# Kernel tuning notes

Measured on AMD Instinct MI355X. Metric: run time of the kernel, lower is better.

The kernel has to match this reference:

```python
import jax, jax.numpy as jnp
import numpy as np

B, P, ENC, DEC, ATT, EMB, V, MEM, TCAP = 64, 196, 2048, 512, 512, 512, 10000, 128, 22
T = TCAP - 1  # max decode length (caption_lengths - 1)


def setup_inputs() -> dict:
    key = jax.random.key(0)
    ks = iter(jax.random.split(key, 32))
    def w(shape, s=0.02):
        return (jax.random.normal(next(ks), shape, jnp.float32) * s)
    encoder_out = jax.random.normal(next(ks), (B, P, ENC), jnp.float32)
    encoded_captions = jax.random.randint(next(ks), (B, TCAP), 0, V)
    lens = np.sort(np.asarray(jax.random.randint(next(ks), (B,), 5, TCAP + 1)))[::-1].copy()
    lens[0] = TCAP  # ensure max(decode_lengths) == T
    caption_lengths = jnp.asarray(lens, jnp.int32)
    return {
        'encoder_out': encoder_out,
        'encoded_captions': encoded_captions,
        'caption_lengths': caption_lengths,
        'emb_table': w((V, EMB), 0.05),
        # Linear weights stored as [in, out] (torch W.T), so y = x @ W + b
        'W_enc': w((ENC, ATT)), 'b_enc': jnp.zeros((ATT,), jnp.float32),
        'W_dec': w((DEC, ATT)), 'b_dec': jnp.zeros((ATT,), jnp.float32),
        'W_full': w((ATT, 1)), 'b_full': jnp.zeros((1,), jnp.float32),
        'W_inith': w((ENC, DEC)), 'b_inith': jnp.zeros((DEC,), jnp.float32),
        'W_initc': w((ENC, DEC)), 'b_initc': jnp.zeros((DEC,), jnp.float32),
        'W_beta': w((DEC, ENC)), 'b_beta': jnp.zeros((ENC,), jnp.float32),
        # LSTMCell (torch gate order i, f, g, o), stored as [in, 4*dec]
        'W_ih': w((EMB + ENC, 4 * DEC)), 'b_ih': jnp.zeros((4 * DEC,), jnp.float32),
        'W_hh': w((DEC, 4 * DEC)), 'b_hh': jnp.zeros((4 * DEC,), jnp.float32),
        'memory_bank': jax.random.normal(next(ks), (MEM, DEC), jnp.float32),
        'W_fc': w((DEC, V)), 'b_fc': jnp.zeros((V,), jnp.float32),
    }


def _decode(encoder_out, encoded_captions, caption_lengths, emb_table,
            W_enc, b_enc, W_dec, b_dec, W_full, b_full,
            W_inith, b_inith, W_initc, b_initc, W_beta, b_beta,
            W_ih, b_ih, W_hh, b_hh, memory_bank, W_fc, b_fc):
    dec_len = caption_lengths - 1  # decode_lengths
    embs = emb_table[encoded_captions]                 # [B, TCAP, EMB]
    mean_enc = encoder_out.mean(axis=1)                # [B, ENC]
    h0 = mean_enc @ W_inith + b_inith
    c0 = mean_enc @ W_initc + b_initc
    att1 = encoder_out @ W_enc + b_enc                 # [B, P, ATT] precomputed

    x_seq = jnp.swapaxes(embs[:, :T, :], 0, 1)         # [T, B, EMB]
    mask_seq = jnp.arange(T)[:, None] < dec_len[None, :]  # [T, B]

    def step(carry, inp):
        h, c = carry
        x_t, m = inp                                   # [B,EMB], [B]
        # attention
        att2 = h @ W_dec + b_dec                       # [B, ATT]
        e = (jax.nn.relu(att1 + att2[:, None, :]) @ W_full)[..., 0] + b_full[0]  # [B, P]
        alpha = jax.nn.softmax(e, axis=1)
        awe = jnp.einsum('bpe,bp->be', encoder_out, alpha)  # [B, ENC]
        gate = jax.nn.sigmoid(h @ W_beta + b_beta)
        awe = gate * awe
        # LSTMCell
        xi = jnp.concatenate([x_t, awe], axis=1)
        gates = xi @ W_ih + b_ih + h @ W_hh + b_hh      # [B, 4*DEC]
        gi, gf, gg, go = jnp.split(gates, 4, axis=1)
        c_new = jax.nn.sigmoid(gf) * c + jax.nn.sigmoid(gi) * jnp.tanh(gg)
        h_new = jax.nn.sigmoid(go) * jnp.tanh(c_new)
        # hash memory
        sim = h_new @ memory_bank.T                    # [B, MEM]
        h_new = h_new + jax.nn.softmax(sim, axis=1) @ memory_bank
        # fc (dropout = identity in eval)
        preds = h_new @ W_fc + b_fc                    # [B, V]
        m2 = m[:, None]
        h = jnp.where(m2, h_new, h)
        c = jnp.where(m2, c_new, c)
        preds = jnp.where(m2, preds, 0.0)
        alpha = jnp.where(m2, alpha, 0.0)
        return (h, c), (preds, alpha)

    (_, _), (preds_seq, alpha_seq) = jax.lax.scan(step, (h0, c0), (x_seq, mask_seq))
    predictions = jnp.swapaxes(preds_seq, 0, 1)        # [B, T, V]
    alphas = jnp.swapaxes(alpha_seq, 0, 1)             # [B, T, P]
    return predictions, dec_len, alphas


def reference(encoder_out, encoded_captions, caption_lengths, emb_table,
              W_enc, b_enc, W_dec, b_dec, W_full, b_full,
              W_inith, b_inith, W_initc, b_initc, W_beta, b_beta,
              W_ih, b_ih, W_hh, b_hh, memory_bank, W_fc, b_fc):
    return _decode(encoder_out, encoded_captions, caption_lengths, emb_table,
                   W_enc, b_enc, W_dec, b_dec, W_full, b_full,
                   W_inith, b_inith, W_initc, b_initc, W_beta, b_beta,
                   W_ih, b_ih, W_hh, b_hh, memory_bank, W_fc, b_fc)
```

## Files before the change

kernel.cpp:

```cpp
#include <hip/hip_runtime.h>

#define BB   64
#define PP   196
#define ENCD 2048
#define DECD 512
#define VV   10000
#define TT   21
#define KIH  2560

typedef __attribute__((ext_vector_type(8))) short bf16x8;
typedef __attribute__((ext_vector_type(4))) float f32x4;

__device__ __forceinline__ float sigm(float x)   { return 1.f / (1.f + __expf(-x)); }
__device__ __forceinline__ float tanh_f(float x) { return 1.f - 2.f / (1.f + __expf(2.f * x)); }
__device__ __forceinline__ ushort f2bf(float x) {
    unsigned u = __float_as_uint(x);
    unsigned r = (u + 0x7FFFu + ((u >> 16) & 1u)) >> 16;
    return (ushort)r;
}
__device__ __forceinline__ float bf2f(short u) {
    return __uint_as_float(((unsigned)(ushort)u) << 16);
}
union U8 { float4 f4; ushort u[8]; };


__global__ void k_cvt(const float* __restrict__ in, ushort* __restrict__ out, int n4) {
    int i = blockIdx.x * 256 + threadIdx.x;
    if (i >= n4) return;
    float4 v = ((const float4*)in)[i];
    ushort4 o; o.x = f2bf(v.x); o.y = f2bf(v.y); o.z = f2bf(v.z); o.w = f2bf(v.w);
    ((ushort4*)out)[i] = o;
}

__global__ void k_mean16(const ushort* __restrict__ encB, float* __restrict__ mean) {
    int idx = blockIdx.x * 256 + threadIdx.x;
    int b = idx >> 10, e2 = idx & 1023;
    const uint* p = (const uint*)encB + (size_t)b * PP * 1024 + e2;
    float s0 = 0.f, s1 = 0.f;
    #pragma unroll 7
    for (int i = 0; i < PP; ++i) {
        uint v = p[(size_t)i * 1024];
        s0 += __uint_as_float(v << 16);
        s1 += __uint_as_float(v & 0xffff0000u);
    }
    mean[b * 2048 + e2 * 2]     = s0 * (1.f / 196.f);
    mean[b * 2048 + e2 * 2 + 1] = s1 * (1.f / 196.f);
}

__global__ __launch_bounds__(256) void k_ipart(const float* __restrict__ mean,
        const float* __restrict__ Wh, const float* __restrict__ Wc,
        float* __restrict__ ipart) {
    __shared__ alignas(16) float As[32][68];
    __shared__ alignas(16) float Bs[32][68];
    const int n0 = blockIdx.x * 64;
    const int kc = blockIdx.y;
    const int mat = blockIdx.z;
    const float* Bp = mat ? Wc : Wh;
    const int tid = threadIdx.x, tx = tid & 15, ty = tid >> 4;
    float acc[4][4] = {};
    for (int k0 = 0; k0 < 512; k0 += 32) {
        #pragma unroll
        for (int p = 0; p < 2; ++p) {
            int c = p * 256 + tid;
            int m = c >> 3, k4 = (c & 7) * 4;
            float4 v = *(const float4*)(mean + m * 2048 + kc * 512 + k0 + k4);
            As[k4 + 0][m] = v.x; As[k4 + 1][m] = v.y; As[k4 + 2][m] = v.z; As[k4 + 3][m] = v.w;
            int kb = c >> 4, n4 = (c & 15) * 4;
            float4 w = *(const float4*)(Bp + (size_t)(kc * 512 + k0 + kb) * 512 + n0 + n4);
            *(float4*)&Bs[kb][n4] = w;
        }
        __syncthreads();
        #pragma unroll 8
        for (int k = 0; k < 32; ++k) {
            float4 a = *(const float4*)&As[k][ty * 4];
            float4 b = *(const float4*)&Bs[k][tx * 4];
            float av[4] = {a.x, a.y, a.z, a.w}, bv[4] = {b.x, b.y, b.z, b.w};
            #pragma unroll
            for (int i = 0; i < 4; ++i)
                #pragma unroll
                for (int j = 0; j < 4; ++j) acc[i][j] += av[i] * bv[j];
        }
        __syncthreads();
    }
    #pragma unroll
    for (int i = 0; i < 4; ++i) {
        int m = ty * 4 + i;
        #pragma unroll
        for (int j = 0; j < 4; ++j) {
            int n = n0 + tx * 4 + j;
            ipart[((size_t)(mat * 4 + kc) * BB + m) * 512 + n] = acc[i][j];
        }
    }
}

__global__ void k_ifin(const float* __restrict__ ipart,
                       const float* __restrict__ bh, const float* __restrict__ bc,
                       float* __restrict__ h, float* __restrict__ c, ushort* __restrict__ hB) {
    int idx = blockIdx.x * 256 + threadIdx.x;
    int mat = idx >> 15, rem = idx & 32767;
    int b = rem >> 9, d = rem & 511;
    float s = 0.f;
    #pragma unroll
    for (int kc = 0; kc < 4; ++kc) s += ipart[((size_t)(mat * 4 + kc) * BB + b) * 512 + d];
    if (mat) c[rem] = s + bc[d];
    else { float v = s + bh[d]; h[rem] = v; hB[rem] = f2bf(v); }
}

__global__ __launch_bounds__(256) void k_tcvt_all(
        const float* __restrict__ Wenc, const float* __restrict__ Wdec,
        const float* __restrict__ Wbeta, const float* __restrict__ Whh,
        const float* __restrict__ Wih, const float* __restrict__ Wfc,
        ushort* __restrict__ WencT, ushort* __restrict__ WdecT,
        ushort* __restrict__ WbetaT, ushort* __restrict__ WhhT,
        ushort* __restrict__ WihT, ushort* __restrict__ WfcT) {
    __shared__ float lds[64 * 65];
    int l = blockIdx.x;
    const float* in; ushort* out; int K, N, KT;
    if (l < 256)       { in = Wenc;  out = WencT;  K = 2048; N = 512;   KT = 32; }
    else if (l < 320)  { l -= 256;  in = Wdec;  out = WdecT;  K = 512;  N = 512;   KT = 8; }
    else if (l < 576)  { l -= 320;  in = Wbeta; out = WbetaT; K = 512;  N = 2048;  KT = 8; }
    else if (l < 832)  { l -= 576;  in = Whh;   out = WhhT;   K = 512;  N = 2048;  KT = 8; }
    else if (l < 2112) { l -= 832;  in = Wih;   out = WihT;   K = KIH;  N = 2048;  KT = 40; }
    else               { l -= 2112; in = Wfc;   out = WfcT;   K = 512;  N = 10000; KT = 8; }
    const int k0 = (l % KT) * 64, n0 = (l / KT) * 64;
    const int tid = threadIdx.x;
    for (int i = tid; i < 4096; i += 256) {
        int kk = i >> 6, nn = i & 63;
        float v = 0.f;
        if (n0 + nn < N) v = in[(size_t)(k0 + kk) * N + n0 + nn];
        lds[nn * 65 + kk] = v;
    }
    __syncthreads();
    for (int i = tid; i < 4096; i += 256) {
        int nn = i >> 6, kk = i & 63;
        out[(size_t)(n0 + nn) * K + k0 + kk] = f2bf(lds[nn * 65 + kk]);
    }
}

__global__ __launch_bounds__(256) void k_att1_256(const ushort* __restrict__ A,
        const ushort* __restrict__ Bt, const float* __restrict__ bias,
        ushort* __restrict__ C) {
    __shared__ alignas(16) ushort As[64 * 64];
    __shared__ alignas(16) ushort Bs[256 * 64];
    const int n0 = blockIdx.x * 256;
    const int m0 = blockIdx.y * 64;
    const int tid = threadIdx.x, wid = tid >> 6, lane = tid & 63;
    f32x4 acc[4][4] = {};
    for (int k0 = 0; k0 < 2048; k0 += 64) {
        #pragma unroll
        for (int p = 0; p < 2; ++p) {
            int c = p * 256 + tid;
            int r = c >> 3, cc = c & 7;
            float4 v = *(const float4*)(A + (size_t)(m0 + r) * 2048 + k0 + cc * 8);
            *(float4*)(As + r * 64 + ((cc ^ (r & 7)) * 8)) = v;
        }
        #pragma unroll
        for (int p = 0; p < 8; ++p) {
            int c = p * 256 + tid;
            int r = c >> 3, cc = c & 7;
            float4 v = *(const float4*)(Bt + (size_t)(n0 + r) * 2048 + k0 + cc * 8);
            *(float4*)(Bs + r * 64 + ((cc ^ (r & 7)) * 8)) = v;
        }
        __syncthreads();
        #pragma unroll
        for (int kk = 0; kk < 2; ++kk) {
            int ci = kk * 4 + (lane >> 4);
            bf16x8 afrag[4], bfrag[4];
            #pragma unroll
            for (int m = 0; m < 4; ++m) {
                int row = m * 16 + (lane & 15);
                afrag[m] = *(const bf16x8*)(As + row * 64 + ((ci ^ (row & 7)) * 8));
            }
            #pragma unroll
            for (int n = 0; n < 4; ++n) {
                int col = wid * 64 + n * 16 + (lane & 15);
                bfrag[n] = *(const bf16x8*)(Bs + col * 64 + ((ci ^ (col & 7)) * 8));
            }
            #pragma unroll
            for (int m = 0; m < 4; ++m)
                #pragma unroll
                for (int n = 0; n < 4; ++n)
                    acc[m][n] = __builtin_amdgcn_mfma_f32_16x16x32_bf16(afrag[m], bfrag[n], acc[m][n], 0, 0, 0);
        }
        __syncthreads();
    }
    #pragma unroll
    for (int m = 0; m < 4; ++m) {
        int rb = m0 + m * 16 + (lane >> 4) * 4;
        #pragma unroll
        for (int n = 0; n < 4; ++n) {
            int col = n0 + wid * 64 + n * 16 + (lane & 15);
            float bv = bias[col];
            #pragma unroll
            for (int r = 0; r < 4; ++r)
                C[(size_t)(rb + r) * 512 + col] = f2bf(acc[m][n][r] + bv);
        }
    }
}

__global__ void k_declen(const int* __restrict__ lens, float* __restrict__ out) {
    int b = threadIdx.x;
    if (b < BB) out[b] = (float)(lens[b] - 1);
}


__global__ __launch_bounds__(256) void k_hgemm64(const ushort* __restrict__ hB,
        const float* __restrict__ emb, const int* __restrict__ caps, int t,
        const ushort* __restrict__ WdecT, const float* __restrict__ bd,
        const ushort* __restrict__ WbetaT, const float* __restrict__ bb,
        const ushort* __restrict__ WhhT, const ushort* __restrict__ WihT,
        float* __restrict__ att2, float* __restrict__ gate, float* __restrict__ hhp) {
    __shared__ alignas(16) ushort As[64 * 64];
    __shared__ alignas(16) ushort Bs[64 * 64];
    __shared__ int capsh[64];
    const int bx = blockIdx.x;
    int seg, n0;
    if (bx < 8)       { seg = 0; n0 = bx * 64; }
    else if (bx < 40) { seg = 1; n0 = (bx - 8) * 64; }
    else              { seg = 2; n0 = (bx - 40) * 64; }
    const int tid = threadIdx.x, wid = tid >> 6, lane = tid & 63;
    if (tid < 64) capsh[tid] = caps[tid * 22 + t];
    __syncthreads();
    const int KSEG = (seg == 2) ? 1024 : 512;
    f32x4 acc[4] = {};
    for (int k0 = 0; k0 < KSEG; k0 += 64) {
        const bool second = k0 >= 512;
        #pragma unroll
        for (int p = 0; p < 2; ++p) {
            int c = p * 256 + tid;
            int r = c >> 3, cc = c & 7;
            if (!second) {
                float4 v = *(const float4*)(hB + r * 512 + k0 + cc * 8);
                *(float4*)(As + r * 64 + ((cc ^ (r & 7)) * 8)) = v;
            } else {
                const float* er = emb + (size_t)capsh[r] * 512 + (k0 - 512) + cc * 8;
                float4 v0 = *(const float4*)er;
                float4 v1 = *(const float4*)(er + 4);
                U8 pk;
                pk.u[0] = f2bf(v0.x); pk.u[1] = f2bf(v0.y); pk.u[2] = f2bf(v0.z); pk.u[3] = f2bf(v0.w);
                pk.u[4] = f2bf(v1.x); pk.u[5] = f2bf(v1.y); pk.u[6] = f2bf(v1.z); pk.u[7] = f2bf(v1.w);
                *(float4*)(As + r * 64 + ((cc ^ (r & 7)) * 8)) = pk.f4;
            }
            const ushort* brow;
            if (seg == 0)      brow = WdecT + (size_t)(n0 + r) * 512 + k0 + cc * 8;
            else if (seg == 1) brow = WbetaT + (size_t)(n0 + r) * 512 + k0 + cc * 8;
            else brow = second ? (WihT + (size_t)(n0 + r) * KIH + (k0 - 512) + cc * 8)
                               : (WhhT + (size_t)(n0 + r) * 512 + k0 + cc * 8);
            float4 v = *(const float4*)brow;
            *(float4*)(Bs + r * 64 + ((cc ^ (r & 7)) * 8)) = v;
        }
        __syncthreads();
        #pragma unroll
        for (int kk = 0; kk < 2; ++kk) {
            int ci = kk * 4 + (lane >> 4);
            int colL = wid * 16 + (lane & 15);
            bf16x8 bfrag = *(const bf16x8*)(Bs + colL * 64 + ((ci ^ (colL & 7)) * 8));
            #pragma unroll
            for (int m = 0; m < 4; ++m) {
                int row = m * 16 + (lane & 15);
                bf16x8 afrag = *(const bf16x8*)(As + row * 64 + ((ci ^ (row & 7)) * 8));
                acc[m] = __builtin_amdgcn_mfma_f32_16x16x32_bf16(afrag, bfrag, acc[m], 0, 0, 0);
            }
        }
        __syncthreads();
    }
    int colL = wid * 16 + (lane & 15);
    int col = n0 + colL;
    #pragma unroll
    for (int m = 0; m < 4; ++m) {
        int rb = m * 16 + (lane >> 4) * 4;
        #pragma unroll
        for (int r = 0; r < 4; ++r) {
            int row = rb + r;
            float v = acc[m][r];
            if (seg == 0)      att2[row * 512 + col] = v + bd[col];
            else if (seg == 1) gate[row * 2048 + col] = sigm(v + bb[col]);
            else               hhp[(size_t)row * 2048 + col] = v;
        }
    }
}

__global__ __launch_bounds__(256) void k_escore_p(const ushort* __restrict__ att1B,
        const float* __restrict__ att2, const float* __restrict__ Wf,
        float* __restrict__ es) {
    __shared__ float a2[512], wf[512];
    int b = blockIdx.y, pc = blockIdx.x, tid = threadIdx.x;
    for (int i = tid; i < 512; i += 256) { a2[i] = att2[b * 512 + i]; wf[i] = Wf[i]; }
    __syncthreads();
    int lane = tid & 63, wid = tid >> 6;
    for (int i = wid; i < 49; i += 4) {
        int p = pc * 49 + i;
        bf16x8 rv = *(const bf16x8*)(att1B + ((size_t)(b * PP + p)) * 512 + lane * 8);
        float s = 0.f;
        #pragma unroll
        for (int j = 0; j < 8; ++j) {
            float v = bf2f(rv[j]) + a2[lane * 8 + j];
            s += (v > 0.f ? v : 0.f) * wf[lane * 8 + j];
        }
        #pragma unroll
        for (int off = 32; off; off >>= 1) s += __shfl_down(s, off);
        if (lane == 0) es[b * 256 + p] = s;
    }
}

__global__ __launch_bounds__(256) void k_awe16s(const ushort* __restrict__ encB,
        const float* __restrict__ es, const float* __restrict__ gate,
        const int* __restrict__ lens, int t,
        uint* __restrict__ aweB, float* __restrict__ out_alpha) {
    __shared__ float al[224], red[256];
    int b = blockIdx.y, pc = blockIdx.x, tid = threadIdx.x;
    float v = (tid < PP) ? es[b * 256 + tid] : -3.4e38f;
    red[tid] = v; __syncthreads();
    for (int s = 128; s; s >>= 1) { if (tid < s) red[tid] = fmaxf(red[tid], red[tid + s]); __syncthreads(); }
    float mx = red[0]; __syncthreads();
    float ev = (tid < PP) ? __expf(v - mx) : 0.f;
    red[tid] = ev; __syncthreads();
    for (int s = 128; s; s >>= 1) { if (tid < s) red[tid] += red[tid + s]; __syncthreads(); }
    float inv = 1.f / red[0];
    if (tid < PP) {
        float a = ev * inv;
        al[tid] = a;
        if (pc == 0) {
            bool m = t < (lens[b] - 1);
            out_alpha[((size_t)b * TT + t) * PP + tid] = m ? a : 0.f;
        }
    }
    __syncthreads();
    int pair = pc * 128 + (tid >> 1);
    int half = tid & 1;
    const uint* p = (const uint*)encB + (size_t)b * PP * 1024 + pair;
    float s0 = 0.f, s1 = 0.f;
    int i0 = half * 98;
    #pragma unroll 7
    for (int i = i0; i < i0 + 98; ++i) {
        uint vv = p[(size_t)i * 1024];
        float a = al[i];
        s0 += a * __uint_as_float(vv << 16);
        s1 += a * __uint_as_float(vv & 0xffff0000u);
    }
    s0 += __shfl_xor(s0, 1);
    s1 += __shfl_xor(s1, 1);
    if (half == 0) {
        int e = pair * 2;
        float g0 = s0 * gate[b * 2048 + e];
        float g1 = s1 * gate[b * 2048 + e + 1];
        aweB[b * 1024 + pair] = (uint)f2bf(g0) | ((uint)f2bf(g1) << 16);
    }
}

__global__ __launch_bounds__(256) void k_gawe64(const ushort* __restrict__ aweB,
        const ushort* __restrict__ WihT, float* __restrict__ pawe) {
    __shared__ alignas(16) ushort As[64 * 64];
    __shared__ alignas(16) ushort Bs[64 * 64];
    const int n0 = blockIdx.x * 64;
    const int kc = blockIdx.y;
    const int tid = threadIdx.x, wid = tid >> 6, lane = tid & 63;
    f32x4 acc[4] = {};
    for (int k0 = 0; k0 < 512; k0 += 64) {
        #pragma unroll
        for (int p = 0; p < 2; ++p) {
            int c = p * 256 + tid;
            int r = c >> 3, cc = c & 7;
            float4 v = *(const float4*)(aweB + r * 2048 + kc * 512 + k0 + cc * 8);
            *(float4*)(As + r * 64 + ((cc ^ (r & 7)) * 8)) = v;
            float4 w = *(const float4*)(WihT + (size_t)(n0 + r) * KIH + 512 + kc * 512 + k0 + cc * 8);
            *(float4*)(Bs + r * 64 + ((cc ^ (r & 7)) * 8)) = w;
        }
        __syncthreads();
        #pragma unroll
        for (int kk = 0; kk < 2; ++kk) {
            int ci = kk * 4 + (lane >> 4);
            int colL = wid * 16 + (lane & 15);
            bf16x8 bfrag = *(const bf16x8*)(Bs + colL * 64 + ((ci ^ (colL & 7)) * 8));
            #pragma unroll
            for (int m = 0; m < 4; ++m) {
                int row = m * 16 + (lane & 15);
                bf16x8 afrag = *(const bf16x8*)(As + row * 64 + ((ci ^ (row & 7)) * 8));
                acc[m] = __builtin_amdgcn_mfma_f32_16x16x32_bf16(afrag, bfrag, acc[m], 0, 0, 0);
            }
        }
        __syncthreads();
    }
    int col = n0 + wid * 16 + (lane & 15);
    #pragma unroll
    for (int m = 0; m < 4; ++m) {
        int rb = m * 16 + (lane >> 4) * 4;
        #pragma unroll
        for (int r = 0; r < 4; ++r)
            pawe[((size_t)kc * BB + rb + r) * 2048 + col] = acc[m][r];
    }
}

__global__ __launch_bounds__(256) void k_memattn(const float* __restrict__ hhp,
        const float* __restrict__ pawe,
        const float* __restrict__ bih, const float* __restrict__ bhh,
        const int* __restrict__ lens, int t, const float* __restrict__ memB,
        float* __restrict__ h, float* __restrict__ c,
        ushort* __restrict__ hB, ushort* __restrict__ histB) {
    __shared__ float hs[512], sims[128], red[256], ps[128];
    int b = blockIdx.x, tid = threadIdx.x;
    bool msk = t < (lens[b] - 1);
    for (int j = tid; j < 512; j += 256) {
        float g[4];
        #pragma unroll
        for (int q = 0; q < 4; ++q) {
            int col = q * 512 + j;
            float s = bih[col] + bhh[col] + hhp[(size_t)b * 2048 + col];
            #pragma unroll
            for (int kc = 0; kc < 4; ++kc) s += pawe[((size_t)kc * BB + b) * 2048 + col];
            g[q] = s;
        }
        float gi = sigm(g[0]), gf = sigm(g[1]), gg = tanh_f(g[2]), go = sigm(g[3]);
        float cold = c[b * 512 + j];
        float cn = gf * cold + gi * gg;
        c[b * 512 + j] = msk ? cn : cold;
        hs[j] = go * tanh_f(cn);
    }
    __syncthreads();
    int lane = tid & 63, wid = tid >> 6;
    for (int m = wid * 32; m < wid * 32 + 32; ++m) {
        const float* r = memB + (size_t)m * 512 + lane * 8;
        float4 r0 = *(const float4*)(r);
        float4 r1 = *(const float4*)(r + 4);
        float4 h0 = *(const float4*)(&hs[lane * 8]);
        float4 h1 = *(const float4*)(&hs[lane * 8 + 4]);
        float s = r0.x * h0.x + r0.y * h0.y + r0.z * h0.z + r0.w * h0.w
                + r1.x * h1.x + r1.y * h1.y + r1.z * h1.z + r1.w * h1.w;
        #pragma unroll
        for (int off = 32; off; off >>= 1) s += __shfl_down(s, off);
        if (lane == 0) sims[m] = s;
    }
    __syncthreads();
    float v = (tid < 128) ? sims[tid] : -3.4e38f;
    red[tid] = v; __syncthreads();
    for (int s = 128; s; s >>= 1) { if (tid < s) red[tid] = fmaxf(red[tid], red[tid + s]); __syncthreads(); }
    float mx = red[0]; __syncthreads();
    float ev = (tid < 128) ? __expf(v - mx) : 0.f;
    red[tid] = ev; __syncthreads();
    for (int s = 128; s; s >>= 1) { if (tid < s) red[tid] += red[tid + s]; __syncthreads(); }
    if (tid < 128) ps[tid] = ev / red[0];
    __syncthreads();
    for (int d = tid; d < 512; d += 256) {
        float s = 0.f;
        #pragma unroll 4
        for (int m = 0; m < 128; ++m) s += ps[m] * memB[(size_t)m * 512 + d];
        float hn = hs[d] + s;
        histB[((size_t)t * BB + b) * 512 + d] = f2bf(hn);
        float hold = h[b * 512 + d];
        float hv = msk ? hn : hold;
        h[b * 512 + d] = hv;
        hB[b * 512 + d] = f2bf(hv);
    }
}

__global__ __launch_bounds__(256) void k_preds_batch(const ushort* __restrict__ histB,
        const ushort* __restrict__ WfcT, const float* __restrict__ bfc,
        const int* __restrict__ lens, float* __restrict__ out) {
    __shared__ alignas(16) ushort As[64 * 64];
    __shared__ alignas(16) ushort Bs[256 * 64];
    const int n0 = blockIdx.x * 256;
    const int t = blockIdx.y;
    const ushort* A = histB + (size_t)t * BB * 512;
    const int tid = threadIdx.x, wid = tid >> 6, lane = tid & 63;
    f32x4 acc[4][4] = {};
    for (int k0 = 0; k0 < 512; k0 += 64) {
        #pragma unroll
        for (int p = 0; p < 2; ++p) {
            int c = p * 256 + tid;
            int r = c >> 3, cc = c & 7;
            float4 v = *(const float4*)(A + r * 512 + k0 + cc * 8);
            *(float4*)(As + r * 64 + ((cc ^ (r & 7)) * 8)) = v;
        }
        #pragma unroll
        for (int p = 0; p < 8; ++p) {
            int c = p * 256 + tid;
            int r = c >> 3, cc = c & 7;
            float4 v = *(const float4*)(WfcT + (size_t)(n0 + r) * 512 + k0 + cc * 8);
            *(float4*)(Bs + r * 64 + ((cc ^ (r & 7)) * 8)) = v;
        }
        __syncthreads();
        #pragma unroll
        for (int kk = 0; kk < 2; ++kk) {
            int ci = kk * 4 + (lane >> 4);
            bf16x8 afrag[4], bfrag[4];
            #pragma unroll
            for (int m = 0; m < 4; ++m) {
                int row = m * 16 + (lane & 15);
                afrag[m] = *(const bf16x8*)(As + row * 64 + ((ci ^ (row & 7)) * 8));
            }
            #pragma unroll
            for (int n = 0; n < 4; ++n) {
                int col = wid * 64 + n * 16 + (lane & 15);
                bfrag[n] = *(const bf16x8*)(Bs + col * 64 + ((ci ^ (col & 7)) * 8));
            }
            #pragma unroll
            for (int m = 0; m < 4; ++m)
                #pragma unroll
                for (int n = 0; n < 4; ++n)
                    acc[m][n] = __builtin_amdgcn_mfma_f32_16x16x32_bf16(afrag[m], bfrag[n], acc[m][n], 0, 0, 0);
        }
        __syncthreads();
    }
    #pragma unroll
    for (int m = 0; m < 4; ++m) {
        int rb = m * 16 + (lane >> 4) * 4;
        #pragma unroll
        for (int n = 0; n < 4; ++n) {
            int col = n0 + wid * 64 + n * 16 + (lane & 15);
            if (col < VV) {
                float bv = bfc[col];
                #pragma unroll
                for (int r = 0; r < 4; ++r) {
                    int b = rb + r;
                    bool msk = t < (lens[b] - 1);
                    out[((size_t)b * TT + t) * VV + col] = msk ? (acc[m][n][r] + bv) : 0.f;
                }
            }
        }
    }
}


extern "C" void kernel_launch(void* const* d_in, const int* in_sizes, int n_in,
                              void* d_out, int out_size, void* d_ws, size_t ws_size,
                              hipStream_t stream) {
    const float* enc     = (const float*)d_in[0];
    const int*   caps    = (const int*)d_in[1];
    const int*   lens    = (const int*)d_in[2];
    const float* emb     = (const float*)d_in[3];
    const float* W_enc   = (const float*)d_in[4];
    const float* b_enc   = (const float*)d_in[5];
    const float* W_dec   = (const float*)d_in[6];
    const float* b_dec   = (const float*)d_in[7];
    const float* W_full  = (const float*)d_in[8];
    const float* W_inith = (const float*)d_in[10];
    const float* b_inith = (const float*)d_in[11];
    const float* W_initc = (const float*)d_in[12];
    const float* b_initc = (const float*)d_in[13];
    const float* W_beta  = (const float*)d_in[14];
    const float* b_beta  = (const float*)d_in[15];
    const float* W_ih    = (const float*)d_in[16];
    const float* b_ih    = (const float*)d_in[17];
    const float* W_hh    = (const float*)d_in[18];
    const float* b_hh    = (const float*)d_in[19];
    const float* memB    = (const float*)d_in[20];
    const float* W_fc    = (const float*)d_in[21];
    const float* b_fc    = (const float*)d_in[22];

    float* out = (float*)d_out;
    float* preds_out  = out;
    float* declen_out = out + (size_t)BB * TT * VV;
    float* alpha_out  = declen_out + BB;

    float* ws    = (float*)d_ws;
    ushort* att1B = (ushort*)ws;        ws += (size_t)12544 * 512 / 2;
    float* h     = ws;  ws += BB * DECD;
    float* c     = ws;  ws += BB * DECD;
    float* att2  = ws;  ws += BB * 512;
    float* gate  = ws;  ws += BB * ENCD;
    float* es    = ws;  ws += BB * 256;
    float* hhp   = ws;  ws += BB * 2048;
    float* pawe  = ws;  ws += (size_t)4 * BB * 2048;
    ushort* hB   = (ushort*)ws;  ws += BB * DECD / 2;
    uint*  aweB  = (uint*)ws;    ws += BB * ENCD / 2;
    ushort* histB = (ushort*)ws; ws += (size_t)TT * BB * DECD / 2;
    ushort* encB  = (ushort*)ws; ws += (size_t)12544 * 2048 / 2;
    ushort* WencT = (ushort*)ws; ws += (size_t)512 * 2048 / 2;
    ushort* WfcT  = (ushort*)ws; ws += (size_t)10240 * 512 / 2;
    ushort* WdecT = (ushort*)ws; ws += (size_t)512 * 512 / 2;
    ushort* WbetaT= (ushort*)ws; ws += (size_t)2048 * 512 / 2;
    ushort* WhhT  = (ushort*)ws; ws += (size_t)2048 * 512 / 2;
    ushort* WihT  = (ushort*)ws; ws += (size_t)2048 * KIH / 2;
    float* ipart = hhp;
    float* mean  = (float*)att1B;

    k_cvt<<<(12544 * 2048 / 4 + 255) / 256, 256, 0, stream>>>(enc, encB, 12544 * 2048 / 4);
    k_mean16<<<256, 256, 0, stream>>>(encB, mean);
    k_ipart<<<dim3(8, 4, 2), 256, 0, stream>>>(mean, W_inith, W_initc, ipart);
    k_ifin<<<256, 256, 0, stream>>>(ipart, b_inith, b_initc, h, c, hB);
    k_declen<<<1, 64, 0, stream>>>(lens, declen_out);
    k_tcvt_all<<<3392, 256, 0, stream>>>(W_enc, W_dec, W_beta, W_hh, W_ih, W_fc,
                                         WencT, WdecT, WbetaT, WhhT, WihT, WfcT);
    k_att1_256<<<dim3(2, 196), 256, 0, stream>>>(encB, WencT, b_enc, att1B);

    for (int t = 0; t < TT; ++t) {
        k_hgemm64<<<72, 256, 0, stream>>>(hB, emb, caps, t, WdecT, b_dec, WbetaT, b_beta,
                                          WhhT, WihT, att2, gate, hhp);
        k_escore_p<<<dim3(4, 64), 256, 0, stream>>>(att1B, att2, W_full, es);
        k_awe16s<<<dim3(8, 64), 256, 0, stream>>>(encB, es, gate, lens, t, aweB, alpha_out);
        k_gawe64<<<dim3(32, 4), 256, 0, stream>>>((const ushort*)aweB, WihT, pawe);
        k_memattn<<<64, 256, 0, stream>>>(hhp, pawe, b_ih, b_hh, lens, t, memB, h, c, hB, histB);
    }
    k_preds_batch<<<dim3(40, TT), 256, 0, stream>>>(histB, WfcT, b_fc, lens, preds_out);
}
```

Before: 1.965 ms.

## Fuse per-step decode kernels into one cooperative persistent kernel with grid sync

Replaces the five per-timestep kernel launches with one cooperative persistent kernel that runs all 21 steps, separated by grid-wide syncs, and keeps a launch-per-phase fallback. The embedding part of the LSTM input projection is hoisted into a batched GEMM over all timesteps before the loop. The Wdec/Wbeta/Whh weights are concatenated into a single GEMM. att1 is stored transposed so the score and softmax/awe phases can be fused per batch row. The aim is to remove launch overhead and redundant per-step work. The cost is four grid barriers per step and a serial 512-length score loop per thread.

```diff
diff --git a/kernel.cpp b/kernel.cpp
--- a/kernel.cpp
+++ b/kernel.cpp
@@ -1,4 +1,7 @@
 #include <hip/hip_runtime.h>
+#include <hip/hip_cooperative_groups.h>
+
+namespace cg = cooperative_groups;
 
 #define BB   64
 #define PP   196
@@ -18,8 +21,8 @@
     unsigned r = (u + 0x7FFFu + ((u >> 16) & 1u)) >> 16;
     return (ushort)r;
 }
-__device__ __forceinline__ float bf2f(short u) {
-    return __uint_as_float(((unsigned)(ushort)u) << 16);
+__device__ __forceinline__ float bf2f(ushort u) {
+    return __uint_as_float(((unsigned)u) << 16);
 }
 union U8 { float4 f4; ushort u[8]; };
 
@@ -137,9 +140,9 @@
     }
 }
 
-__global__ __launch_bounds__(256) void k_att1_256(const ushort* __restrict__ A,
+__global__ __launch_bounds__(256) void k_att1T(const ushort* __restrict__ A,
         const ushort* __restrict__ Bt, const float* __restrict__ bias,
-        ushort* __restrict__ C) {
+        ushort* __restrict__ att1T) {
     __shared__ alignas(16) ushort As[64 * 64];
     __shared__ alignas(16) ushort Bs[256 * 64];
     const int n0 = blockIdx.x * 256;
@@ -187,13 +190,86 @@
     #pragma unroll
     for (int m = 0; m < 4; ++m) {
         int rb = m0 + m * 16 + (lane >> 4) * 4;
+        int b = rb / 196;
+        int p = rb - b * 196;
         #pragma unroll
         for (int n = 0; n < 4; ++n) {
             int col = n0 + wid * 64 + n * 16 + (lane & 15);
             float bv = bias[col];
+            ushort4 o;
+            o.x = f2bf(acc[m][n][0] + bv);
+            o.y = f2bf(acc[m][n][1] + bv);
+            o.z = f2bf(acc[m][n][2] + bv);
+            o.w = f2bf(acc[m][n][3] + bv);
+            *(ushort4*)(att1T + ((size_t)(b * 512 + col)) * 200 + p) = o;
+        }
+    }
+}
+
+__global__ __launch_bounds__(256) void k_xpre(const float* __restrict__ emb,
+        const int* __restrict__ caps, const ushort* __restrict__ WihT,
+        float* __restrict__ xpre) {
+    __shared__ alignas(16) ushort As[64 * 64];
+    __shared__ alignas(16) ushort Bs[256 * 64];
+    __shared__ int capsh[64];
+    const int n0 = blockIdx.x * 256;
+    const int t = blockIdx.y;
+    const int tid = threadIdx.x, wid = tid >> 6, lane = tid & 63;
+    if (tid < 64) capsh[tid] = caps[tid * 22 + t];
+    __syncthreads();
+    f32x4 acc[4][4] = {};
+    for (int k0 = 0; k0 < 512; k0 += 64) {
+        #pragma unroll
+        for (int p = 0; p < 2; ++p) {
+            int c = p * 256 + tid;
+            int r = c >> 3, cc = c & 7;
+            const float* er = emb + (size_t)capsh[r] * 512 + k0 + cc * 8;
+            float4 v0 = *(const float4*)er;
+            float4 v1 = *(const float4*)(er + 4);
+            U8 pk;
+            pk.u[0] = f2bf(v0.x); pk.u[1] = f2bf(v0.y); pk.u[2] = f2bf(v0.z); pk.u[3] = f2bf(v0.w);
+            pk.u[4] = f2bf(v1.x); pk.u[5] = f2bf(v1.y); pk.u[6] = f2bf(v1.z); pk.u[7] = f2bf(v1.w);
+            *(float4*)(As + r * 64 + ((cc ^ (r & 7)) * 8)) = pk.f4;
+        }
+        #pragma unroll
+        for (int p = 0; p < 8; ++p) {
+            int c = p * 256 + tid;
+            int r = c >> 3, cc = c & 7;
+            float4 v = *(const float4*)(WihT + (size_t)(n0 + r) * KIH + k0 + cc * 8);
+            *(float4*)(Bs + r * 64 + ((cc ^ (r & 7)) * 8)) = v;
+        }
+        __syncthreads();
+        #pragma unroll
+        for (int kk = 0; kk < 2; ++kk) {
+            int ci = kk * 4 + (lane >> 4);
+            bf16x8 afrag[4], bfrag[4];
+            #pragma unroll
+            for (int m = 0; m < 4; ++m) {
+                int row = m * 16 + (lane & 15);
+                afrag[m] = *(const bf16x8*)(As + row * 64 + ((ci ^ (row & 7)) * 8));
+            }
+            #pragma unroll
+            for (int n = 0; n < 4; ++n) {
+                int col = wid * 64 + n * 16 + (lane & 15);
+                bfrag[n] = *(const bf16x8*)(Bs + col * 64 + ((ci ^ (col & 7)) * 8));
+            }
+            #pragma unroll
+            for (int m = 0; m < 4; ++m)
+                #pragma unroll
+                for (int n = 0; n < 4; ++n)
+                    acc[m][n] = __builtin_amdgcn_mfma_f32_16x16x32_bf16(afrag[m], bfrag[n], acc[m][n], 0, 0, 0);
+        }
+        __syncthreads();
+    }
+    #pragma unroll
+    for (int m = 0; m < 4; ++m) {
+        int rb = m * 16 + (lane >> 4) * 4;
+        #pragma unroll
+        for (int n = 0; n < 4; ++n) {
+            int col = n0 + wid * 64 + n * 16 + (lane & 15);
             #pragma unroll
             for (int r = 0; r < 4; ++r)
-                C[(size_t)(rb + r) * 512 + col] = f2bf(acc[m][n][r] + bv);
+                xpre[((size_t)t * BB + rb + r) * 2048 + col] = acc[m][n][r];
         }
     }
 }
@@ -204,178 +280,49 @@
 }
 
 
-__global__ __launch_bounds__(256) void k_hgemm64(const ushort* __restrict__ hB,
-        const float* __restrict__ emb, const int* __restrict__ caps, int t,
-        const ushort* __restrict__ WdecT, const float* __restrict__ bd,
-        const ushort* __restrict__ WbetaT, const float* __restrict__ bb,
-        const ushort* __restrict__ WhhT, const ushort* __restrict__ WihT,
-        float* __restrict__ att2, float* __restrict__ gate, float* __restrict__ hhp) {
-    __shared__ alignas(16) ushort As[64 * 64];
-    __shared__ alignas(16) ushort Bs[64 * 64];
-    __shared__ int capsh[64];
-    const int bx = blockIdx.x;
-    int seg, n0;
-    if (bx < 8)       { seg = 0; n0 = bx * 64; }
-    else if (bx < 40) { seg = 1; n0 = (bx - 8) * 64; }
-    else              { seg = 2; n0 = (bx - 40) * 64; }
-    const int tid = threadIdx.x, wid = tid >> 6, lane = tid & 63;
-    if (tid < 64) capsh[tid] = caps[tid * 22 + t];
-    __syncthreads();
-    const int KSEG = (seg == 2) ? 1024 : 512;
+struct SArgs {
+    ushort* hB; float* h; float* c;
+    const ushort* WcatT; const float* bd; const float* bb;
+    const ushort* WihT; const float* xpre; const ushort* att1T;
+    const float* Wf; const ushort* encB;
+    const float* bih; const float* bhh;
+    const int* lens; const float* memB;
+    float* att2; float* gate; float* hhp;
+    uint* aweB; float* pawe;
+    ushort* histB; float* alpha_out;
+};
+
+struct SMem {
+    ushort As[64 * 64];
+    ushort Bs[64 * 64];
+    float a2s[512], wfs[512], reds[256], als[224];
+    float hss[512], simss[128], pss[128];
+};
+
+__device__ __forceinline__ void phase1(const SArgs& a, int bid, int tid, SMem& sm) {
+    const int lane = tid & 63, wid = tid >> 6;
+    const int n0 = bid * 64;
     f32x4 acc[4] = {};
-    for (int k0 = 0; k0 < KSEG; k0 += 64) {
-        const bool second = k0 >= 512;
+    for (int k0 = 0; k0 < 512; k0 += 64) {
         #pragma unroll
         for (int p = 0; p < 2; ++p) {
-            int c = p * 256 + tid;
-            int r = c >> 3, cc = c & 7;
-            if (!second) {
-                float4 v = *(const float4*)(hB + r * 512 + k0 + cc * 8);
-                *(float4*)(As + r * 64 + ((cc ^ (r & 7)) * 8)) = v;
-            } else {
-                const float* er = emb + (size_t)capsh[r] * 512 + (k0 - 512) + cc * 8;
-                float4 v0 = *(const float4*)er;
-                float4 v1 = *(const float4*)(er + 4);
-                U8 pk;
-                pk.u[0] = f2bf(v0.x); pk.u[1] = f2bf(v0.y); pk.u[2] = f2bf(v0.z); pk.u[3] = f2bf(v0.w);
-                pk.u[4] = f2bf(v1.x); pk.u[5] = f2bf(v1.y); pk.u[6] = f2bf(v1.z); pk.u[7] = f2bf(v1.w);
-                *(float4*)(As + r * 64 + ((cc ^ (r & 7)) * 8)) = pk.f4;
-            }
-            const ushort* brow;
-            if (seg == 0)      brow = WdecT + (size_t)(n0 + r) * 512 + k0 + cc * 8;
-            else if (seg == 1) brow = WbetaT + (size_t)(n0 + r) * 512 + k0 + cc * 8;
-            else brow = second ? (WihT + (size_t)(n0 + r) * KIH + (k0 - 512) + cc * 8)
-                               : (WhhT + (size_t)(n0 + r) * 512 + k0 + cc * 8);
-            float4 v = *(const float4*)brow;
-            *(float4*)(Bs + r * 64 + ((cc ^ (r & 7)) * 8)) = v;
+            int c8 = p * 256 + tid;
+            int r = c8 >> 3, cc = c8 & 7;
+            float4 v = *(const float4*)(a.hB + r * 512 + k0 + cc * 8);
+            *(float4*)(sm.As + r * 64 + ((cc ^ (r & 7)) * 8)) = v;
+            float4 w = *(const float4*)(a.WcatT + (size_t)(n0 + r) * 512 + k0 + cc * 8);
+            *(float4*)(sm.Bs + r * 64 + ((cc ^ (r & 7)) * 8)) = w;
         }
         __syncthreads();
         #pragma unroll
         for (int kk = 0; kk < 2; ++kk) {
             int ci = kk * 4 + (lane >> 4);
             int colL = wid * 16 + (lane & 15);
-            bf16x8 bfrag = *(const bf16x8*)(Bs + colL * 64 + ((ci ^ (colL & 7)) * 8));
+            bf16x8 bfrag = *(const bf16x8*)(sm.Bs + colL * 64 + ((ci ^ (colL & 7)) * 8));
             #pragma unroll
             for (int m = 0; m < 4; ++m) {
                 int row = m * 16 + (lane & 15);
-                bf16x8 afrag = *(const bf16x8*)(As + row * 64 + ((ci ^ (row & 7)) * 8));
-                acc[m] = __builtin_amdgcn_mfma_f32_16x16x32_bf16(afrag, bfrag, acc[m], 0, 0, 0);
-            }
-        }
-        __syncthreads();
-    }
-    int colL = wid * 16 + (lane & 15);
-    int col = n0 + colL;
-    #pragma unroll
-    for (int m = 0; m < 4; ++m) {
-        int rb = m * 16 + (lane >> 4) * 4;
-        #pragma unroll
-        for (int r = 0; r < 4; ++r) {
-            int row = rb + r;
-            float v = acc[m][r];
-            if (seg == 0)      att2[row * 512 + col] = v + bd[col];
-            else if (seg == 1) gate[row * 2048 + col] = sigm(v + bb[col]);
-            else               hhp[(size_t)row * 2048 + col] = v;
-        }
-    }
-}
-
-__global__ __launch_bounds__(256) void k_escore_p(const ushort* __restrict__ att1B,
-        const float* __restrict__ att2, const float* __restrict__ Wf,
-        float* __restrict__ es) {
-    __shared__ float a2[512], wf[512];
-    int b = blockIdx.y, pc = blockIdx.x, tid = threadIdx.x;
-    for (int i = tid; i < 512; i += 256) { a2[i] = att2[b * 512 + i]; wf[i] = Wf[i]; }
-    __syncthreads();
-    int lane = tid & 63, wid = tid >> 6;
-    for (int i = wid; i < 49; i += 4) {
-        int p = pc * 49 + i;
-        bf16x8 rv = *(const bf16x8*)(att1B + ((size_t)(b * PP + p)) * 512 + lane * 8);
-        float s = 0.f;
-        #pragma unroll
-        for (int j = 0; j < 8; ++j) {
-            float v = bf2f(rv[j]) + a2[lane * 8 + j];
-            s += (v > 0.f ? v : 0.f) * wf[lane * 8 + j];
-        }
-        #pragma unroll
-        for (int off = 32; off; off >>= 1) s += __shfl_down(s, off);
-        if (lane == 0) es[b * 256 + p] = s;
-    }
-}
-
-__global__ __launch_bounds__(256) void k_awe16s(const ushort* __restrict__ encB,
-        const float* __restrict__ es, const float* __restrict__ gate,
-        const int* __restrict__ lens, int t,
-        uint* __restrict__ aweB, float* __restrict__ out_alpha) {
-    __shared__ float al[224], red[256];
-    int b = blockIdx.y, pc = blockIdx.x, tid = threadIdx.x;
-    float v = (tid < PP) ? es[b * 256 + tid] : -3.4e38f;
-    red[tid] = v; __syncthreads();
-    for (int s = 128; s; s >>= 1) { if (tid < s) red[tid] = fmaxf(red[tid], red[tid + s]); __syncthreads(); }
-    float mx = red[0]; __syncthreads();
-    float ev = (tid < PP) ? __expf(v - mx) : 0.f;
-    red[tid] = ev; __syncthreads();
-    for (int s = 128; s; s >>= 1) { if (tid < s) red[tid] += red[tid + s]; __syncthreads(); }
-    float inv = 1.f / red[0];
-    if (tid < PP) {
-        float a = ev * inv;
-        al[tid] = a;
-        if (pc == 0) {
-            bool m = t < (lens[b] - 1);
-            out_alpha[((size_t)b * TT + t) * PP + tid] = m ? a : 0.f;
-        }
-    }
-    __syncthreads();
-    int pair = pc * 128 + (tid >> 1);
-    int half = tid & 1;
-    const uint* p = (const uint*)encB + (size_t)b * PP * 1024 + pair;
-    float s0 = 0.f, s1 = 0.f;
-    int i0 = half * 98;
-    #pragma unroll 7
-    for (int i = i0; i < i0 + 98; ++i) {
-        uint vv = p[(size_t)i * 1024];
-        float a = al[i];
-        s0 += a * __uint_as_float(vv << 16);
-        s1 += a * __uint_as_float(vv & 0xffff0000u);
-    }
-    s0 += __shfl_xor(s0, 1);
-    s1 += __shfl_xor(s1, 1);
-    if (half == 0) {
-        int e = pair * 2;
-        float g0 = s0 * gate[b * 2048 + e];
-        float g1 = s1 * gate[b * 2048 + e + 1];
-        aweB[b * 1024 + pair] = (uint)f2bf(g0) | ((uint)f2bf(g1) << 16);
-    }
-}
-
-__global__ __launch_bounds__(256) void k_gawe64(const ushort* __restrict__ aweB,
-        const ushort* __restrict__ WihT, float* __restrict__ pawe) {
-    __shared__ alignas(16) ushort As[64 * 64];
-    __shared__ alignas(16) ushort Bs[64 * 64];
-    const int n0 = blockIdx.x * 64;
-    const int kc = blockIdx.y;
-    const int tid = threadIdx.x, wid = tid >> 6, lane = tid & 63;
-    f32x4 acc[4] = {};
-    for (int k0 = 0; k0 < 512; k0 += 64) {
-        #pragma unroll
-        for (int p = 0; p < 2; ++p) {
-            int c = p * 256 + tid;
-            int r = c >> 3, cc = c & 7;
-            float4 v = *(const float4*)(aweB + r * 2048 + kc * 512 + k0 + cc * 8);
-            *(float4*)(As + r * 64 + ((cc ^ (r & 7)) * 8)) = v;
-            float4 w = *(const float4*)(WihT + (size_t)(n0 + r) * KIH + 512 + kc * 512 + k0 + cc * 8);
-            *(float4*)(Bs + r * 64 + ((cc ^ (r & 7)) * 8)) = w;
-        }
-        __syncthreads();
-        #pragma unroll
-        for (int kk = 0; kk < 2; ++kk) {
-            int ci = kk * 4 + (lane >> 4);
-            int colL = wid * 16 + (lane & 15);
-            bf16x8 bfrag = *(const bf16x8*)(Bs + colL * 64 + ((ci ^ (colL & 7)) * 8));
-            #pragma unroll
-            for (int m = 0; m < 4; ++m) {
-                int row = m * 16 + (lane & 15);
-                bf16x8 afrag = *(const bf16x8*)(As + row * 64 + ((ci ^ (row & 7)) * 8));
+                bf16x8 afrag = *(const bf16x8*)(sm.As + row * 64 + ((ci ^ (row & 7)) * 8));
                 acc[m] = __builtin_amdgcn_mfma_f32_16x16x32_bf16(afrag, bfrag, acc[m], 0, 0, 0);
             }
         }
@@ -386,71 +333,188 @@
     for (int m = 0; m < 4; ++m) {
         int rb = m * 16 + (lane >> 4) * 4;
         #pragma unroll
+        for (int r = 0; r < 4; ++r) {
+            int row = rb + r;
+            float v = acc[m][r];
+            if (col < 512)       a.att2[row * 512 + col] = v + a.bd[col];
+            else if (col < 2560) a.gate[row * 2048 + (col - 512)] = sigm(v + a.bb[col - 512]);
+            else                 a.hhp[(size_t)row * 2048 + (col - 2560)] = v;
+        }
+    }
+}
+
+__device__ __forceinline__ void phase2(const SArgs& a, int t, int bid, int tid, SMem& sm) {
+    const int b = bid >> 2, pc = bid & 3;
+    for (int i = tid; i < 512; i += 256) { sm.a2s[i] = a.att2[b * 512 + i]; sm.wfs[i] = a.Wf[i]; }
+    __syncthreads();
+    float es = -3.4e38f;
+    if (tid < PP) {
+        const ushort* rp = a.att1T + (size_t)b * 512 * 200 + tid;
+        float s = 0.f;
+        #pragma unroll 4
+        for (int k = 0; k < 512; ++k) {
+            float v = bf2f(rp[(size_t)k * 200]) + sm.a2s[k];
+            s += (v > 0.f ? v : 0.f) * sm.wfs[k];
+        }
+        es = s;
+    }
+    sm.reds[tid] = es; __syncthreads();
+    for (int s = 128; s; s >>= 1) { if (tid < s) sm.reds[tid] = fmaxf(sm.reds[tid], sm.reds[tid + s]); __syncthreads(); }
+    float mx = sm.reds[0]; __syncthreads();
+    float ev = (tid < PP) ? __expf(es - mx) : 0.f;
+    sm.reds[tid] = ev; __syncthreads();
+    for (int s = 128; s; s >>= 1) { if (tid < s) sm.reds[tid] += sm.reds[tid + s]; __syncthreads(); }
+    float inv = 1.f / sm.reds[0];
+    if (tid < PP) {
+        float al = ev * inv;
+        sm.als[tid] = al;
+        if (pc == 0) {
+            bool m = t < (a.lens[b] - 1);
+            a.alpha_out[((size_t)b * TT + t) * PP + tid] = m ? al : 0.f;
+        }
+    }
+    __syncthreads();
+    int pair = pc * 256 + tid;
+    const uint* pp = (const uint*)a.encB + (size_t)b * PP * 1024 + pair;
+    float s0 = 0.f, s1 = 0.f;
+    #pragma unroll 4
+    for (int i = 0; i < PP; ++i) {
+        uint vv = pp[(size_t)i * 1024];
+        float al = sm.als[i];
+        s0 += al * __uint_as_float(vv << 16);
+        s1 += al * __uint_as_float(vv & 0xffff0000u);
+    }
+    int e = pair * 2;
+    float g0 = s0 * a.gate[b * 2048 + e];
+    float g1 = s1 * a.gate[b * 2048 + e + 1];
+    a.aweB[b * 1024 + pair] = (uint)f2bf(g0) | ((uint)f2bf(g1) << 16);
+}
+
+__device__ __forceinline__ void phase3(const SArgs& a, int bid, int tid, SMem& sm) {
+    const int lane = tid & 63, wid = tid >> 6;
+    const int n0 = (bid & 31) * 64, kc = bid >> 5;
+    const ushort* aweU = (const ushort*)a.aweB;
+    f32x4 acc[4] = {};
+    for (int k0 = 0; k0 < 512; k0 += 64) {
+        #pragma unroll
+        for (int p = 0; p < 2; ++p) {
+            int c8 = p * 256 + tid;
+            int r = c8 >> 3, cc = c8 & 7;
+            float4 v = *(const float4*)(aweU + r * 2048 + kc * 512 + k0 + cc * 8);
+            *(float4*)(sm.As + r * 64 + ((cc ^ (r & 7)) * 8)) = v;
+            float4 w = *(const float4*)(a.WihT + (size_t)(n0 + r) * KIH + 512 + kc * 512 + k0 + cc * 8);
+            *(float4*)(sm.Bs + r * 64 + ((cc ^ (r & 7)) * 8)) = w;
+        }
+        __syncthreads();
+        #pragma unroll
+        for (int kk = 0; kk < 2; ++kk) {
+            int ci = kk * 4 + (lane >> 4);
+            int colL = wid * 16 + (lane & 15);
+            bf16x8 bfrag = *(const bf16x8*)(sm.Bs + colL * 64 + ((ci ^ (colL & 7)) * 8));
+            #pragma unroll
+            for (int m = 0; m < 4; ++m) {
+                int row = m * 16 + (lane & 15);
+                bf16x8 afrag = *(const bf16x8*)(sm.As + row * 64 + ((ci ^ (row & 7)) * 8));
+                acc[m] = __builtin_amdgcn_mfma_f32_16x16x32_bf16(afrag, bfrag, acc[m], 0, 0, 0);
+            }
+        }
+        __syncthreads();
+    }
+    int col = n0 + wid * 16 + (lane & 15);
+    #pragma unroll
+    for (int m = 0; m < 4; ++m) {
+        int rb = m * 16 + (lane >> 4) * 4;
+        #pragma unroll
         for (int r = 0; r < 4; ++r)
-            pawe[((size_t)kc * BB + rb + r) * 2048 + col] = acc[m][r];
-    }
-}
-
-__global__ __launch_bounds__(256) void k_memattn(const float* __restrict__ hhp,
-        const float* __restrict__ pawe,
-        const float* __restrict__ bih, const float* __restrict__ bhh,
-        const int* __restrict__ lens, int t, const float* __restrict__ memB,
-        float* __restrict__ h, float* __restrict__ c,
-        ushort* __restrict__ hB, ushort* __restrict__ histB) {
-    __shared__ float hs[512], sims[128], red[256], ps[128];
-    int b = blockIdx.x, tid = threadIdx.x;
-    bool msk = t < (lens[b] - 1);
+            a.pawe[((size_t)kc * BB + rb + r) * 2048 + col] = acc[m][r];
+    }
+}
+
+__device__ __forceinline__ void phase4(const SArgs& a, int t, int bid, int tid, SMem& sm) {
+    const int lane = tid & 63, wid = tid >> 6;
+    const int b = bid;
+    bool msk = t < (a.lens[b] - 1);
     for (int j = tid; j < 512; j += 256) {
         float g[4];
         #pragma unroll
         for (int q = 0; q < 4; ++q) {
             int col = q * 512 + j;
-            float s = bih[col] + bhh[col] + hhp[(size_t)b * 2048 + col];
-            #pragma unroll
-            for (int kc = 0; kc < 4; ++kc) s += pawe[((size_t)kc * BB + b) * 2048 + col];
+            float s = a.bih[col] + a.bhh[col]
+                    + a.hhp[(size_t)b * 2048 + col]
+                    + a.xpre[((size_t)t * BB + b) * 2048 + col];
+            #pragma unroll
+            for (int kc = 0; kc < 4; ++kc) s += a.pawe[((size_t)kc * BB + b) * 2048 + col];
             g[q] = s;
         }
         float gi = sigm(g[0]), gf = sigm(g[1]), gg = tanh_f(g[2]), go = sigm(g[3]);
-        float cold = c[b * 512 + j];
+        float cold = a.c[b * 512 + j];
         float cn = gf * cold + gi * gg;
-        c[b * 512 + j] = msk ? cn : cold;
-        hs[j] = go * tanh_f(cn);
+        a.c[b * 512 + j] = msk ? cn : cold;
+        sm.hss[j] = go * tanh_f(cn);
     }
     __syncthreads();
-    int lane = tid & 63, wid = tid >> 6;
     for (int m = wid * 32; m < wid * 32 + 32; ++m) {
-        const float* r = memB + (size_t)m * 512 + lane * 8;
+        const float* r = a.memB + (size_t)m * 512 + lane * 8;
         float4 r0 = *(const float4*)(r);
         float4 r1 = *(const float4*)(r + 4);
-        float4 h0 = *(const float4*)(&hs[lane * 8]);
-        float4 h1 = *(const float4*)(&hs[lane * 8 + 4]);
+        float4 h0 = *(const float4*)(&sm.hss[lane * 8]);
+        float4 h1 = *(const float4*)(&sm.hss[lane * 8 + 4]);
         float s = r0.x * h0.x + r0.y * h0.y + r0.z * h0.z + r0.w * h0.w
                 + r1.x * h1.x + r1.y * h1.y + r1.z * h1.z + r1.w * h1.w;
         #pragma unroll
         for (int off = 32; off; off >>= 1) s += __shfl_down(s, off);
-        if (lane == 0) sims[m] = s;
+        if (lane == 0) sm.simss[m] = s;
     }
     __syncthreads();
-    float v = (tid < 128) ? sims[tid] : -3.4e38f;
-    red[tid] = v; __syncthreads();
-    for (int s = 128; s; s >>= 1) { if (tid < s) red[tid] = fmaxf(red[tid], red[tid + s]); __syncthreads(); }
-    float mx = red[0]; __syncthreads();
+    float v = (tid < 128) ? sm.simss[tid] : -3.4e38f;
+    sm.reds[tid] = v; __syncthreads();
+    for (int s = 128; s; s >>= 1) { if (tid < s) sm.reds[tid] = fmaxf(sm.reds[tid], sm.reds[tid + s]); __syncthreads(); }
+    float mx = sm.reds[0]; __syncthreads();
     float ev = (tid < 128) ? __expf(v - mx) : 0.f;
-    red[tid] = ev; __syncthreads();
-    for (int s = 128; s; s >>= 1) { if (tid < s) red[tid] += red[tid + s]; __syncthreads(); }
-    if (tid < 128) ps[tid] = ev / red[0];
+    sm.reds[tid] = ev; __syncthreads();
+    for (int s = 128; s; s >>= 1) { if (tid < s) sm.reds[tid] += sm.reds[tid + s]; __syncthreads(); }
+    if (tid < 128) sm.pss[tid] = ev / sm.reds[0];
     __syncthreads();
     for (int d = tid; d < 512; d += 256) {
         float s = 0.f;
         #pragma unroll 4
-        for (int m = 0; m < 128; ++m) s += ps[m] * memB[(size_t)m * 512 + d];
-        float hn = hs[d] + s;
-        histB[((size_t)t * BB + b) * 512 + d] = f2bf(hn);
-        float hold = h[b * 512 + d];
+        for (int m = 0; m < 128; ++m) s += sm.pss[m] * a.memB[(size_t)m * 512 + d];
+        float hn = sm.hss[d] + s;
+        a.histB[((size_t)t * BB + b) * 512 + d] = f2bf(hn);
+        float hold = a.h[b * 512 + d];
         float hv = msk ? hn : hold;
-        h[b * 512 + d] = hv;
-        hB[b * 512 + d] = f2bf(hv);
-    }
+        a.h[b * 512 + d] = hv;
+        a.hB[b * 512 + d] = f2bf(hv);
+    }
+}
+
+__global__ __launch_bounds__(256) void k_steps(SArgs a) {
+    cg::grid_group grid = cg::this_grid();
+    __shared__ SMem sm;
+    const int bid = blockIdx.x, tid = threadIdx.x;
+    for (int t = 0; t < TT; ++t) {
+        if (bid < 72) phase1(a, bid, tid, sm);
+        grid.sync();
+        phase2(a, t, bid, tid, sm);
+        grid.sync();
+        if (bid < 128) phase3(a, bid, tid, sm);
+        grid.sync();
+        if (bid < 64) phase4(a, t, bid, tid, sm);
+        grid.sync();
+    }
+}
+
+__global__ __launch_bounds__(256) void k_p1(SArgs a) {
+    __shared__ SMem sm; phase1(a, blockIdx.x, threadIdx.x, sm);
+}
+__global__ __launch_bounds__(256) void k_p2(SArgs a, int t) {
+    __shared__ SMem sm; phase2(a, t, blockIdx.x, threadIdx.x, sm);
+}
+__global__ __launch_bounds__(256) void k_p3(SArgs a) {
+    __shared__ SMem sm; phase3(a, blockIdx.x, threadIdx.x, sm);
+}
+__global__ __launch_bounds__(256) void k_p4(SArgs a, int t) {
+    __shared__ SMem sm; phase4(a, t, blockIdx.x, threadIdx.x, sm);
 }
 
 __global__ __launch_bounds__(256) void k_preds_batch(const ushort* __restrict__ histB,
@@ -553,26 +617,24 @@
     float* alpha_out  = declen_out + BB;
 
     float* ws    = (float*)d_ws;
-    ushort* att1B = (ushort*)ws;        ws += (size_t)12544 * 512 / 2;
+    ushort* att1T = (ushort*)ws;  ws += (size_t)64 * 512 * 200 / 2;
     float* h     = ws;  ws += BB * DECD;
     float* c     = ws;  ws += BB * DECD;
     float* att2  = ws;  ws += BB * 512;
-    float* gate  = ws;  ws += BB * ENCD;
-    float* es    = ws;  ws += BB * 256;
+    float* gate  = ws;  ws += BB * 2048;
     float* hhp   = ws;  ws += BB * 2048;
     float* pawe  = ws;  ws += (size_t)4 * BB * 2048;
+    float* xpre  = ws;  ws += (size_t)TT * BB * 2048;
     ushort* hB   = (ushort*)ws;  ws += BB * DECD / 2;
-    uint*  aweB  = (uint*)ws;    ws += BB * ENCD / 2;
+    uint*  aweB  = (uint*)ws;    ws += BB * 1024;
     ushort* histB = (ushort*)ws; ws += (size_t)TT * BB * DECD / 2;
     ushort* encB  = (ushort*)ws; ws += (size_t)12544 * 2048 / 2;
     ushort* WencT = (ushort*)ws; ws += (size_t)512 * 2048 / 2;
     ushort* WfcT  = (ushort*)ws; ws += (size_t)10240 * 512 / 2;
-    ushort* WdecT = (ushort*)ws; ws += (size_t)512 * 512 / 2;
-    ushort* WbetaT= (ushort*)ws; ws += (size_t)2048 * 512 / 2;
-    ushort* WhhT  = (ushort*)ws; ws += (size_t)2048 * 512 / 2;
+    ushort* WcatT = (ushort*)ws; ws += (size_t)4608 * 512 / 2;
     ushort* WihT  = (ushort*)ws; ws += (size_t)2048 * KIH / 2;
-    float* ipart = hhp;
-    float* mean  = (float*)att1B;
+    float* mean  = (float*)att1T;
+    float* ipart = xpre;
 
     k_cvt<<<(12544 * 2048 / 4 + 255) / 256, 256, 0, stream>>>(enc, encB, 12544 * 2048 / 4);
     k_mean16<<<256, 256, 0, stream>>>(encB, mean);
@@ -580,16 +642,34 @@
     k_ifin<<<256, 256, 0, stream>>>(ipart, b_inith, b_initc, h, c, hB);
     k_declen<<<1, 64, 0, stream>>>(lens, declen_out);
     k_tcvt_all<<<3392, 256, 0, stream>>>(W_enc, W_dec, W_beta, W_hh, W_ih, W_fc,
-                                         WencT, WdecT, WbetaT, WhhT, WihT, WfcT);
-    k_att1_256<<<dim3(2, 196), 256, 0, stream>>>(encB, WencT, b_enc, att1B);
-
-    for (int t = 0; t < TT; ++t) {
-        k_hgemm64<<<72, 256, 0, stream>>>(hB, emb, caps, t, WdecT, b_dec, WbetaT, b_beta,
-                                          WhhT, WihT, att2, gate, hhp);
-        k_escore_p<<<dim3(4, 64), 256, 0, stream>>>(att1B, att2, W_full, es);
-        k_awe16s<<<dim3(8, 64), 256, 0, stream>>>(encB, es, gate, lens, t, aweB, alpha_out);
-        k_gawe64<<<dim3(32, 4), 256, 0, stream>>>((const ushort*)aweB, WihT, pawe);
-        k_memattn<<<64, 256, 0, stream>>>(hhp, pawe, b_ih, b_hh, lens, t, memB, h, c, hB, histB);
-    }
+                                         WencT, WcatT, WcatT + (size_t)512 * 512,
+                                         WcatT + (size_t)2560 * 512, WihT, WfcT);
+    k_att1T<<<dim3(2, 196), 256, 0, stream>>>(encB, WencT, b_enc, att1T);
+    k_xpre<<<dim3(8, TT), 256, 0, stream>>>(emb, caps, WihT, xpre);
+
+    SArgs sa;
+    sa.hB = hB; sa.h = h; sa.c = c;
+    sa.WcatT = WcatT; sa.bd = b_dec; sa.bb = b_beta;
+    sa.WihT = WihT; sa.xpre = xpre; sa.att1T = att1T;
+    sa.Wf = W_full; sa.encB = encB;
+    sa.bih = b_ih; sa.bhh = b_hh;
+    sa.lens = lens; sa.memB = memB;
+    sa.att2 = att2; sa.gate = gate; sa.hhp = hhp;
+    sa.aweB = aweB; sa.pawe = pawe;
+    sa.histB = histB; sa.alpha_out = alpha_out;
+
+    void* kargs[] = { (void*)&sa };
+    hipError_t ce = hipLaunchCooperativeKernel((const void*)k_steps, dim3(256), dim3(256),
+                                               kargs, 0, stream);
+    if (ce != hipSuccess) {
+        (void)hipGetLastError();
+        for (int t = 0; t < TT; ++t) {
+            k_p1<<<72,  256, 0, stream>>>(sa);
+            k_p2<<<256, 256, 0, stream>>>(sa, t);
+            k_p3<<<128, 256, 0, stream>>>(sa);
+            k_p4<<<64,  256, 0, stream>>>(sa, t);
+        }
+    }
+
     k_preds_batch<<<dim3(40, TT), 256, 0, stream>>>(histB, WfcT, b_fc, lens, preds_out);
 }
```

Result: slower. 4.938 ms (+151.3%).
